# Kernel optimization log

Hardware: AMD Instinct MI355X
Metric: run time of the kernel (lower is better)

## Reference

```python
import jax, jax.numpy as jnp
import numpy as np

N_NODES = 100000


def gcn_conv(x, src, dst, W, b, n_nodes):
    # PyG GCNConv: add self-loops, sym-normalize, transform then aggregate.
    loop = jnp.arange(n_nodes, dtype=src.dtype)
    s = jnp.concatenate([src, loop])
    d = jnp.concatenate([dst, loop])
    ones = jnp.ones(s.shape[0], dtype=x.dtype)
    deg = jax.ops.segment_sum(ones, d, num_segments=n_nodes)
    dinv = jnp.where(deg > 0, jax.lax.rsqrt(deg), 0.0)
    norm = dinv[s] * dinv[d]  # [E+N]
    h = x @ W                 # [N, out]
    msg = h[s] * norm[:, None]
    out = jax.ops.segment_sum(msg, d, num_segments=n_nodes)
    return out + b


def setup_inputs() -> dict:
    key = jax.random.key(0)
    ks = jax.random.split(key, 10)
    n, f = N_NODES, 128
    x = jax.random.normal(ks[0], (n, f), dtype=jnp.float32)
    edge_index = jax.random.randint(ks[1], (2, 1600000), 0, n, dtype=jnp.int64)

    def glorot(k, fin, fout):
        lim = float(np.sqrt(6.0 / (fin + fout)))
        return jax.random.uniform(k, (fin, fout), jnp.float32, -lim, lim)

    return {
        "x": x,
        "edge_index": edge_index,
        "W1": glorot(ks[2], f, 128), "b1": jnp.zeros((128,), jnp.float32),
        "W2": glorot(ks[3], 128, 64), "b2": jnp.zeros((64,), jnp.float32),
        "W3": glorot(ks[4], 64, 32), "b3": jnp.zeros((32,), jnp.float32),
        "Wc": glorot(ks[5], 64, 1), "bc": jnp.zeros((1,), jnp.float32),
    }


def reference(x, edge_index, W1, b1, W2, b2, W3, b3, Wc, bc):
    n = x.shape[0]
    src, dst = edge_index[0], edge_index[1]
    h = jax.nn.relu(gcn_conv(x, src, dst, W1, b1, n))   # dropout: eval mode
    h = jax.nn.relu(gcn_conv(h, src, dst, W2, b2, n))
    h = jax.nn.relu(gcn_conv(h, src, dst, W3, b3, n))
    edge_feat = jnp.concatenate([h[src], h[dst]], axis=1)  # [E, 64]
    return edge_feat @ Wc + bc
```

## Files before the change

### kernel.cpp

```cpp
#include <hip/hip_runtime.h>


typedef unsigned short u16;
typedef short bfrag __attribute__((ext_vector_type(8)));
typedef float ffrag __attribute__((ext_vector_type(4)));

#define BSHIFT 8
#define MAXB   512
#define BIN_CHUNK 4096
#define BCAP   4608

static __device__ __forceinline__ float4 f4add(float4 a, float4 b) {
    return make_float4(a.x + b.x, a.y + b.y, a.z + b.z, a.w + b.w);
}

static __device__ __forceinline__ u16 f2bf(float f) {
    unsigned u = __float_as_uint(f);
    u = (u + 0x7FFFu + ((u >> 16) & 1u)) >> 16;
    return (u16)u;
}

static __device__ __forceinline__ float bflo(unsigned u) {
    return __uint_as_float(u << 16);
}
static __device__ __forceinline__ float bfhi(unsigned u) {
    return __uint_as_float(u & 0xFFFF0000u);
}
static __device__ __forceinline__ void bfacc2(float& a0, float& a1, unsigned u) {
    a0 += bflo(u);
    a1 += bfhi(u);
}


__global__ __launch_bounds__(256) void bin_edges(const int* __restrict__ src,
                                                 const int* __restrict__ dst,
                                                 int* __restrict__ bcur,
                                                 unsigned* __restrict__ pairs,
                                                 int E, int B) {
    __shared__ int h[MAXB];
    __shared__ int base[MAXB];
    const int t = threadIdx.x;
    const int e0 = blockIdx.x * BIN_CHUNK;
    const int eEnd = min(e0 + BIN_CHUNK, E);
    for (int i = t; i < B; i += 256) h[i] = 0;
    __syncthreads();
    for (int e = e0 + t; e < eEnd; e += 256)
        atomicAdd(&h[dst[e] >> BSHIFT], 1);
    __syncthreads();
    for (int i = t; i < B; i += 256) {
        int c = h[i];
        base[i] = c ? atomicAdd(&bcur[i], c) : 0;
        h[i] = 0;
    }
    __syncthreads();
    for (int e = e0 + t; e < eEnd; e += 256) {
        int d = dst[e];
        int b = d >> BSHIFT;
        int pos = base[b] + atomicAdd(&h[b], 1);
        pairs[pos] = ((unsigned)(d & 255) << 24) | (unsigned)src[e];
    }
}

__global__ __launch_bounds__(256) void build_csr(const unsigned* __restrict__ pairs,
                                                 const int* __restrict__ bcur,
                                                 int* __restrict__ rowp,
                                                 int* __restrict__ rowe,
                                                 float* __restrict__ dinv,
                                                 int* __restrict__ ssrc, int N) {
    __shared__ int s[256];
    __shared__ int cur[256];
    const int t = threadIdx.x;
    const int b = blockIdx.x;
    const int eBeg = b * BCAP, eEnd = bcur[b];
    const int nodeBase = b << BSHIFT;
    s[t] = 0;
    __syncthreads();
    for (int e = eBeg + t; e < eEnd; e += 256)
        atomicAdd(&s[pairs[e] >> 24], 1);
    __syncthreads();
    const int v = s[t];
    #pragma unroll
    for (int off = 1; off < 256; off <<= 1) {
        int add = (t >= off) ? s[t - off] : 0;
        __syncthreads();
        s[t] += add;
        __syncthreads();
    }
    const int rp = eBeg + s[t] - v;
    const int node = nodeBase + t;
    if (node < N) {
        rowp[node] = rp;
        rowe[node] = rp + v;
        dinv[node] = rsqrtf((float)(v + 1));
    }
    cur[t] = rp;
    __syncthreads();
    for (int e = eBeg + t; e < eEnd; e += 256) {
        unsigned p = pairs[e];
        int pos = atomicAdd(&cur[p >> 24], 1);
        ssrc[pos] = (int)(p & 0xFFFFFFu);
    }
}

__global__ __launch_bounds__(256) void prep_all(const float* __restrict__ W1,
                                                u16* __restrict__ w1t,
                                                const float* __restrict__ W2,
                                                u16* __restrict__ w2t,
                                                int* __restrict__ bcur, int B) {
    int idx = blockIdx.x * 256 + threadIdx.x;
    if (idx < 128 * 128) {
        int n = idx >> 7, k = idx & 127;
        w1t[idx] = f2bf(W1[k * 128 + n]);
    } else if (idx < 128 * 128 + 64 * 128) {
        int j = idx - 128 * 128;
        int n = j >> 7, k = j & 127;
        w2t[j] = f2bf(W2[k * 64 + n]);
    }
    if (idx < B) bcur[idx] = idx * BCAP;
}

template <int FIN, int FOUT, bool AF32, int MINW>
__global__ __launch_bounds__(256, MINW)
void gemm_mfma(const void* __restrict__ Xv, const u16* __restrict__ Wt,
               const float* __restrict__ dinv, u16* __restrict__ G, int N) {
    constexpr int NT = FOUT / 16;
    constexpr int KK = FIN / 32;
    constexpr int CB = FIN / 8;
    constexpr int ITER = (64 * CB) / 256;
    __shared__ __align__(16) u16 xs[64 * FIN];
    __shared__ float ldv[64];

    const int t = threadIdx.x;
    const int wave = t >> 6;
    const int lane = t & 63;
    const int l15 = lane & 15;
    const int quad = lane >> 4;
    const int r0 = blockIdx.x * 64;

    bfrag Bf[NT][KK];
    #pragma unroll
    for (int nt = 0; nt < NT; nt++)
        #pragma unroll
        for (int kk = 0; kk < KK; kk++)
            Bf[nt][kk] = *reinterpret_cast<const bfrag*>(
                &Wt[(size_t)(nt * 16 + l15) * FIN + kk * 32 + quad * 8]);

    if (t < 64) ldv[t] = (r0 + t < N) ? dinv[r0 + t] : 0.f;

    #pragma unroll
    for (int i = 0; i < ITER; i++) {
        int v = t + 256 * i;
        int row = v / CB;
        int cb = v - row * CB;
        uint4 pack = make_uint4(0, 0, 0, 0);
        if (r0 + row < N) {
            if (AF32) {
                const float* X = (const float*)Xv;
                const float4* p = reinterpret_cast<const float4*>(
                    &X[(size_t)(r0 + row) * FIN + cb * 8]);
                float4 lo = p[0], hi = p[1];
                pack.x = f2bf(lo.x) | ((unsigned)f2bf(lo.y) << 16);
                pack.y = f2bf(lo.z) | ((unsigned)f2bf(lo.w) << 16);
                pack.z = f2bf(hi.x) | ((unsigned)f2bf(hi.y) << 16);
                pack.w = f2bf(hi.z) | ((unsigned)f2bf(hi.w) << 16);
            } else {
                const u16* X = (const u16*)Xv;
                pack = *reinterpret_cast<const uint4*>(
                    &X[(size_t)(r0 + row) * FIN + cb * 8]);
            }
        }
        int cbs = cb ^ (row & 7);
        *reinterpret_cast<uint4*>(&xs[row * FIN + cbs * 8]) = pack;
    }
    __syncthreads();

    ffrag acc[NT];
    #pragma unroll
    for (int nt = 0; nt < NT; nt++) {
        acc[nt][0] = 0.f; acc[nt][1] = 0.f; acc[nt][2] = 0.f; acc[nt][3] = 0.f;
    }

    const int arow = wave * 16 + l15;
    #pragma unroll
    for (int kk = 0; kk < KK; kk++) {
        int cb = (kk * 4 + quad) ^ (l15 & 7);
        bfrag a = *reinterpret_cast<const bfrag*>(&xs[arow * FIN + cb * 8]);
        #pragma unroll
        for (int nt = 0; nt < NT; nt++)
            acc[nt] = __builtin_amdgcn_mfma_f32_16x16x32_bf16(a, Bf[nt][kk], acc[nt], 0, 0, 0);
    }

    #pragma unroll
    for (int nt = 0; nt < NT; nt++)
        #pragma unroll
        for (int r = 0; r < 4; r++) {
            int rl = wave * 16 + quad * 4 + r;
            int grow = r0 + rl;
            if (grow < N)
                G[(size_t)grow * FOUT + nt * 16 + l15] = f2bf(acc[nt][r] * ldv[rl]);
        }
}

__global__ __launch_bounds__(256) void agg1_gemm2(const u16* __restrict__ G,
                                                  const int* __restrict__ rowp,
                                                  const int* __restrict__ rowe,
                                                  const int* __restrict__ ssrc,
                                                  const float* __restrict__ dinv,
                                                  const float* __restrict__ bias,
                                                  const u16* __restrict__ w2t,
                                                  u16* __restrict__ g2, int N) {
    __shared__ __align__(16) u16 hl[16][136];
    __shared__ float ldv[16];
    const int t = threadIdx.x;
    const int wave = t >> 6;
    const int lane = t & 63;
    const int l15 = lane & 15;
    const int quad = lane >> 4;
    const int lj = t & 15;
    const int dn = t >> 4;
    const int d0 = blockIdx.x * 16;
    const int d = d0 + dn;

    bfrag Bf[4];
    #pragma unroll
    for (int kk = 0; kk < 4; kk++)
        Bf[kk] = *reinterpret_cast<const bfrag*>(
            &w2t[(size_t)(wave * 16 + l15) * 128 + kk * 32 + quad * 8]);

    if (t < 16) ldv[t] = (d0 + t < N) ? dinv[d0 + t] : 0.f;

    uint4 pk = make_uint4(0, 0, 0, 0);
    if (d < N) {
        const uint4* G4 = reinterpret_cast<const uint4*>(G);
        float a[8];
        #pragma unroll
        for (int i = 0; i < 8; i++) a[i] = 0.f;
        {
            uint4 u = G4[(size_t)d * 16 + lj];
            bfacc2(a[0], a[1], u.x); bfacc2(a[2], a[3], u.y);
            bfacc2(a[4], a[5], u.z); bfacc2(a[6], a[7], u.w);
        }
        int e = rowp[d];
        const int end = rowe[d];
        for (; e + 4 <= end; e += 4) {
            int s0 = ssrc[e], s1 = ssrc[e + 1], s2 = ssrc[e + 2], s3 = ssrc[e + 3];
            uint4 u0 = G4[(size_t)s0 * 16 + lj];
            uint4 u1 = G4[(size_t)s1 * 16 + lj];
            uint4 u2 = G4[(size_t)s2 * 16 + lj];
            uint4 u3 = G4[(size_t)s3 * 16 + lj];
            bfacc2(a[0], a[1], u0.x); bfacc2(a[2], a[3], u0.y);
            bfacc2(a[4], a[5], u0.z); bfacc2(a[6], a[7], u0.w);
            bfacc2(a[0], a[1], u1.x); bfacc2(a[2], a[3], u1.y);
            bfacc2(a[4], a[5], u1.z); bfacc2(a[6], a[7], u1.w);
            bfacc2(a[0], a[1], u2.x); bfacc2(a[2], a[3], u2.y);
            bfacc2(a[4], a[5], u2.z); bfacc2(a[6], a[7], u2.w);
            bfacc2(a[0], a[1], u3.x); bfacc2(a[2], a[3], u3.y);
            bfacc2(a[4], a[5], u3.z); bfacc2(a[6], a[7], u3.w);
        }
        for (; e < end; e++) {
            uint4 u = G4[(size_t)ssrc[e] * 16 + lj];
            bfacc2(a[0], a[1], u.x); bfacc2(a[2], a[3], u.y);
            bfacc2(a[4], a[5], u.z); bfacc2(a[6], a[7], u.w);
        }
        const float dv = ldv[dn];
        const float4 b0 = reinterpret_cast<const float4*>(bias)[lj * 2];
        const float4 b1 = reinterpret_cast<const float4*>(bias)[lj * 2 + 1];
        float h[8];
        h[0] = fmaxf(a[0] * dv + b0.x, 0.f);
        h[1] = fmaxf(a[1] * dv + b0.y, 0.f);
        h[2] = fmaxf(a[2] * dv + b0.z, 0.f);
        h[3] = fmaxf(a[3] * dv + b0.w, 0.f);
        h[4] = fmaxf(a[4] * dv + b1.x, 0.f);
        h[5] = fmaxf(a[5] * dv + b1.y, 0.f);
        h[6] = fmaxf(a[6] * dv + b1.z, 0.f);
        h[7] = fmaxf(a[7] * dv + b1.w, 0.f);
        pk.x = f2bf(h[0]) | ((unsigned)f2bf(h[1]) << 16);
        pk.y = f2bf(h[2]) | ((unsigned)f2bf(h[3]) << 16);
        pk.z = f2bf(h[4]) | ((unsigned)f2bf(h[5]) << 16);
        pk.w = f2bf(h[6]) | ((unsigned)f2bf(h[7]) << 16);
    }
    *reinterpret_cast<uint4*>(&hl[dn][lj * 8]) = pk;
    __syncthreads();

    ffrag acc;
    acc[0] = 0.f; acc[1] = 0.f; acc[2] = 0.f; acc[3] = 0.f;
    #pragma unroll
    for (int kk = 0; kk < 4; kk++) {
        bfrag av = *reinterpret_cast<const bfrag*>(&hl[l15][kk * 32 + quad * 8]);
        acc = __builtin_amdgcn_mfma_f32_16x16x32_bf16(av, Bf[kk], acc, 0, 0, 0);
    }
    #pragma unroll
    for (int r = 0; r < 4; r++) {
        int row = quad * 4 + r;
        int node = d0 + row;
        if (node < N)
            g2[(size_t)node * 64 + wave * 16 + l15] = f2bf(acc[r] * ldv[row]);
    }
}

__global__ __launch_bounds__(256) void agg2_gemm3(const u16* __restrict__ G,
                                                  const int* __restrict__ rowp,
                                                  const int* __restrict__ rowe,
                                                  const int* __restrict__ ssrc,
                                                  const float* __restrict__ dinv,
                                                  const float* __restrict__ bias,
                                                  const float* __restrict__ W3,
                                                  float* __restrict__ g3, int N) {
    __shared__ __align__(16) float wl[64 * 32];
    __shared__ __align__(16) float hl[32][68];
    const int t = threadIdx.x;
    {
        const float4* s4 = reinterpret_cast<const float4*>(W3);
        float4* d4 = reinterpret_cast<float4*>(wl);
        d4[t] = s4[t];
        d4[t + 256] = s4[t + 256];
    }
    __syncthreads();
    const int lj = t & 7;
    const int dn = t >> 3;
    const int d = blockIdx.x * 32 + dn;
    if (d >= N) return;

    const uint4* G4 = reinterpret_cast<const uint4*>(G);
    float a[8];
    #pragma unroll
    for (int i = 0; i < 8; i++) a[i] = 0.f;
    {
        uint4 u = G4[(size_t)d * 8 + lj];
        bfacc2(a[0], a[1], u.x); bfacc2(a[2], a[3], u.y);
        bfacc2(a[4], a[5], u.z); bfacc2(a[6], a[7], u.w);
    }
    int e = rowp[d];
    const int end = rowe[d];
    for (; e + 4 <= end; e += 4) {
        int s0 = ssrc[e], s1 = ssrc[e + 1], s2 = ssrc[e + 2], s3 = ssrc[e + 3];
        uint4 u0 = G4[(size_t)s0 * 8 + lj];
        uint4 u1 = G4[(size_t)s1 * 8 + lj];
        uint4 u2 = G4[(size_t)s2 * 8 + lj];
        uint4 u3 = G4[(size_t)s3 * 8 + lj];
        bfacc2(a[0], a[1], u0.x); bfacc2(a[2], a[3], u0.y);
        bfacc2(a[4], a[5], u0.z); bfacc2(a[6], a[7], u0.w);
        bfacc2(a[0], a[1], u1.x); bfacc2(a[2], a[3], u1.y);
        bfacc2(a[4], a[5], u1.z); bfacc2(a[6], a[7], u1.w);
        bfacc2(a[0], a[1], u2.x); bfacc2(a[2], a[3], u2.y);
        bfacc2(a[4], a[5], u2.z); bfacc2(a[6], a[7], u2.w);
        bfacc2(a[0], a[1], u3.x); bfacc2(a[2], a[3], u3.y);
        bfacc2(a[4], a[5], u3.z); bfacc2(a[6], a[7], u3.w);
    }
    for (; e < end; e++) {
        uint4 u = G4[(size_t)ssrc[e] * 8 + lj];
        bfacc2(a[0], a[1], u.x); bfacc2(a[2], a[3], u.y);
        bfacc2(a[4], a[5], u.z); bfacc2(a[6], a[7], u.w);
    }
    const float dv = dinv[d];
    const float4 b0 = reinterpret_cast<const float4*>(bias)[lj * 2];
    const float4 b1 = reinterpret_cast<const float4*>(bias)[lj * 2 + 1];
    float h[8];
    h[0] = fmaxf(a[0] * dv + b0.x, 0.f);
    h[1] = fmaxf(a[1] * dv + b0.y, 0.f);
    h[2] = fmaxf(a[2] * dv + b0.z, 0.f);
    h[3] = fmaxf(a[3] * dv + b0.w, 0.f);
    h[4] = fmaxf(a[4] * dv + b1.x, 0.f);
    h[5] = fmaxf(a[5] * dv + b1.y, 0.f);
    h[6] = fmaxf(a[6] * dv + b1.z, 0.f);
    h[7] = fmaxf(a[7] * dv + b1.w, 0.f);
    *reinterpret_cast<float4*>(&hl[dn][lj * 8])     = make_float4(h[0], h[1], h[2], h[3]);
    *reinterpret_cast<float4*>(&hl[dn][lj * 8 + 4]) = make_float4(h[4], h[5], h[6], h[7]);
    float g[4] = {0.f, 0.f, 0.f, 0.f};
    #pragma unroll 4
    for (int k4 = 0; k4 < 16; k4++) {
        float4 hv = *reinterpret_cast<const float4*>(&hl[dn][k4 * 4]);
        float hs[4] = {hv.x, hv.y, hv.z, hv.w};
        #pragma unroll
        for (int p = 0; p < 4; p++) {
            float4 w = *reinterpret_cast<const float4*>(&wl[(k4 * 4 + p) * 32 + lj * 4]);
            g[0] += hs[p] * w.x; g[1] += hs[p] * w.y;
            g[2] += hs[p] * w.z; g[3] += hs[p] * w.w;
        }
    }
    *reinterpret_cast<float4*>(&g3[(size_t)d * 32 + lj * 4]) =
        make_float4(g[0] * dv, g[1] * dv, g[2] * dv, g[3] * dv);
}

__global__ __launch_bounds__(256) void aggregate_l3s(const float* __restrict__ G,
                                                     const int* __restrict__ rowp,
                                                     const int* __restrict__ rowe,
                                                     const int* __restrict__ ssrc,
                                                     const float* __restrict__ dinv,
                                                     const float* __restrict__ bias,
                                                     const float* __restrict__ Wc,
                                                     float2* __restrict__ ab, int N) {
    constexpr int L = 8;
    const int t = threadIdx.x;
    const int lj = t % L;
    const int d = blockIdx.x * 32 + t / L;
    if (d >= N) return;

    const float4* G4 = reinterpret_cast<const float4*>(G);
    float4 acc = G4[(size_t)d * L + lj];
    int e = rowp[d];
    const int end = rowe[d];
    for (; e + 4 <= end; e += 4) {
        int s0 = ssrc[e], s1 = ssrc[e + 1], s2 = ssrc[e + 2], s3 = ssrc[e + 3];
        float4 v0 = G4[(size_t)s0 * L + lj];
        float4 v1 = G4[(size_t)s1 * L + lj];
        float4 v2 = G4[(size_t)s2 * L + lj];
        float4 v3 = G4[(size_t)s3 * L + lj];
        acc = f4add(acc, f4add(f4add(v0, v1), f4add(v2, v3)));
    }
    for (; e < end; e++)
        acc = f4add(acc, G4[(size_t)ssrc[e] * L + lj]);
    const float dv = dinv[d];
    const float4 b4 = reinterpret_cast<const float4*>(bias)[lj];
    float4 h;
    h.x = fmaxf(acc.x * dv + b4.x, 0.f);
    h.y = fmaxf(acc.y * dv + b4.y, 0.f);
    h.z = fmaxf(acc.z * dv + b4.z, 0.f);
    h.w = fmaxf(acc.w * dv + b4.w, 0.f);
    const float4 wa = reinterpret_cast<const float4*>(Wc)[lj];
    const float4 wb = reinterpret_cast<const float4*>(Wc + 32)[lj];
    float p = h.x * wa.x + h.y * wa.y + h.z * wa.z + h.w * wa.w;
    float q = h.x * wb.x + h.y * wb.y + h.z * wb.z + h.w * wb.w;
    p += __shfl_xor(p, 1); q += __shfl_xor(q, 1);
    p += __shfl_xor(p, 2); q += __shfl_xor(q, 2);
    p += __shfl_xor(p, 4); q += __shfl_xor(q, 4);
    if (lj == 0) ab[d] = make_float2(p, q);
}


__global__ __launch_bounds__(256) void edge_out(const int* __restrict__ src,
                                                const int* __restrict__ dst,
                                                const float2* __restrict__ ab,
                                                const float* __restrict__ bc,
                                                float* __restrict__ out, int E) {
    int e = blockIdx.x * 256 + threadIdx.x;
    if (e < E) out[e] = ab[src[e]].x + ab[dst[e]].y + bc[0];
}

extern "C" void kernel_launch(void* const* d_in, const int* in_sizes, int n_in,
                              void* d_out, int out_size, void* d_ws, size_t ws_size,
                              hipStream_t stream) {
    const float* x  = (const float*)d_in[0];
    const int*   ei = (const int*)d_in[1];
    const float* W1 = (const float*)d_in[2];
    const float* b1 = (const float*)d_in[3];
    const float* W2 = (const float*)d_in[4];
    const float* b2 = (const float*)d_in[5];
    const float* W3 = (const float*)d_in[6];
    const float* b3 = (const float*)d_in[7];
    const float* Wc = (const float*)d_in[8];
    const float* bc = (const float*)d_in[9];
    float* out = (float*)d_out;

    const int N = in_sizes[0] / 128;
    const int E = in_sizes[1] / 2;
    const int B = (N + 255) >> BSHIFT;
    const int* src = ei;
    const int* dst = ei + E;

    size_t off = 0;
    auto alloc = [&](size_t bytes) -> void* {
        size_t o = (off + 255) & ~(size_t)255;
        off = o + bytes;
        return (void*)((char*)d_ws + o);
    };
    float* dinv = (float*)alloc((size_t)N * 4);
    int*   rowp = (int*)alloc((size_t)N * 4);
    int*   rowe = (int*)alloc((size_t)N * 4);
    int*   bcur = (int*)alloc((size_t)(B + 1) * 4);
    int*   ssrc = (int*)alloc((size_t)B * BCAP * 4);
    u16*   w1t  = (u16*)alloc(128 * 128 * 2);
    u16*   w2t  = (u16*)alloc(64 * 128 * 2);
    u16*   g16  = (u16*)alloc((size_t)N * 128 * 2);
    u16*   g2b  = (u16*)alloc((size_t)N * 64 * 2);
    float2* ab  = (float2*)alloc((size_t)N * 8);
    (void)ws_size; (void)n_in; (void)out_size;

    unsigned* pairs = (unsigned*)g2b;
    float* g3f = (float*)g16;

    const int gE = (E + 255) / 256;
    const int gR = (N + 63) / 64;

    prep_all<<<96, 256, 0, stream>>>(W1, w1t, W2, w2t, bcur, B);
    bin_edges<<<(E + BIN_CHUNK - 1) / BIN_CHUNK, 256, 0, stream>>>(src, dst, bcur, pairs, E, B);
    build_csr<<<B, 256, 0, stream>>>(pairs, bcur, rowp, rowe, dinv, ssrc, N);

    gemm_mfma<128, 128, true, 2><<<gR, 256, 0, stream>>>(x, w1t, dinv, g16, N);
    agg1_gemm2<<<(N + 15) / 16, 256, 0, stream>>>(g16, rowp, rowe, ssrc, dinv, b1, w2t, g2b, N);
    agg2_gemm3<<<(N + 31) / 32, 256, 0, stream>>>(g2b, rowp, rowe, ssrc, dinv, b2, W3, g3f, N);
    aggregate_l3s<<<(N + 31) / 32, 256, 0, stream>>>(g3f, rowp, rowe, ssrc, dinv, b3, Wc, ab, N);

    edge_out<<<gE, 256, 0, stream>>>(src, dst, ab, bc, out, E);
}
```

Before: 319.8 us.

## Sort nodes by degree within each bin to balance aggregation waves

build_csr now computes a per-bin permutation of nodes, counting-sorted by in-degree with the degree key capped at 63, and writes -1 for padding slots. The three aggregation kernels map each thread group to a node through this permutation, so the threads of one wavefront handle nodes of similar degree and diverge less in their gather loops. The gather loops also gain an 8-way unrolled stage to keep more loads in flight. The cost is an extra indirection load per node, scattered output writes, a serial 64-entry scan on one thread per bin, and higher register pressure from the wider unroll.

```diff
diff --git a/kernel.cpp b/kernel.cpp
--- a/kernel.cpp
+++ b/kernel.cpp
@@ -29,6 +29,10 @@
 static __device__ __forceinline__ void bfacc2(float& a0, float& a1, unsigned u) {
     a0 += bflo(u);
     a1 += bfhi(u);
+}
+static __device__ __forceinline__ void bfacc8(float* a, uint4 u) {
+    bfacc2(a[0], a[1], u.x); bfacc2(a[2], a[3], u.y);
+    bfacc2(a[4], a[5], u.z); bfacc2(a[6], a[7], u.w);
 }
 
 
@@ -66,14 +70,17 @@
                                                  int* __restrict__ rowp,
                                                  int* __restrict__ rowe,
                                                  float* __restrict__ dinv,
-                                                 int* __restrict__ ssrc, int N) {
+                                                 int* __restrict__ ssrc,
+                                                 int* __restrict__ perm, int N) {
     __shared__ int s[256];
     __shared__ int cur[256];
+    __shared__ int hcur[64];
     const int t = threadIdx.x;
     const int b = blockIdx.x;
     const int eBeg = b * BCAP, eEnd = bcur[b];
     const int nodeBase = b << BSHIFT;
     s[t] = 0;
+    if (t < 64) hcur[t] = 0;
     __syncthreads();
     for (int e = eBeg + t; e < eEnd; e += 256)
         atomicAdd(&s[pairs[e] >> 24], 1);
@@ -88,13 +95,28 @@
     }
     const int rp = eBeg + s[t] - v;
     const int node = nodeBase + t;
-    if (node < N) {
+    const int nvalid = min(N - nodeBase, 256);
+    const int dc = min(v, 63);
+    if (t < nvalid) {
         rowp[node] = rp;
         rowe[node] = rp + v;
         dinv[node] = rsqrtf((float)(v + 1));
+        atomicAdd(&hcur[dc], 1);
+    } else {
+        perm[(b << 8) + t] = -1;
     }
     cur[t] = rp;
     __syncthreads();
+    if (t == 0) {
+        int acc = 0;
+        #pragma unroll
+        for (int i = 0; i < 64; i++) { int h = hcur[i]; hcur[i] = acc; acc += h; }
+    }
+    __syncthreads();
+    if (t < nvalid) {
+        int rank = atomicAdd(&hcur[dc], 1);
+        perm[(b << 8) + rank] = node;
+    }
     for (int e = eBeg + t; e < eEnd; e += 256) {
         unsigned p = pairs[e];
         int pos = atomicAdd(&cur[p >> 24], 1);
@@ -205,12 +227,14 @@
                                                   const int* __restrict__ rowp,
                                                   const int* __restrict__ rowe,
                                                   const int* __restrict__ ssrc,
+                                                  const int* __restrict__ perm,
                                                   const float* __restrict__ dinv,
                                                   const float* __restrict__ bias,
                                                   const u16* __restrict__ w2t,
                                                   u16* __restrict__ g2, int N) {
     __shared__ __align__(16) u16 hl[16][136];
     __shared__ float ldv[16];
+    __shared__ int pn[16];
     const int t = threadIdx.x;
     const int wave = t >> 6;
     const int lane = t & 63;
@@ -219,50 +243,48 @@
     const int lj = t & 15;
     const int dn = t >> 4;
     const int d0 = blockIdx.x * 16;
-    const int d = d0 + dn;
-
-    bfrag Bf[4];
-    #pragma unroll
-    for (int kk = 0; kk < 4; kk++)
-        Bf[kk] = *reinterpret_cast<const bfrag*>(
-            &w2t[(size_t)(wave * 16 + l15) * 128 + kk * 32 + quad * 8]);
-
-    if (t < 16) ldv[t] = (d0 + t < N) ? dinv[d0 + t] : 0.f;
+
+    if (t < 16) {
+        int nd = perm[d0 + t];
+        pn[t] = nd;
+        ldv[t] = (nd >= 0) ? dinv[nd] : 0.f;
+    }
+    const int d = perm[d0 + dn];
 
     uint4 pk = make_uint4(0, 0, 0, 0);
-    if (d < N) {
+    if (d >= 0) {
         const uint4* G4 = reinterpret_cast<const uint4*>(G);
         float a[8];
         #pragma unroll
         for (int i = 0; i < 8; i++) a[i] = 0.f;
-        {
-            uint4 u = G4[(size_t)d * 16 + lj];
-            bfacc2(a[0], a[1], u.x); bfacc2(a[2], a[3], u.y);
-            bfacc2(a[4], a[5], u.z); bfacc2(a[6], a[7], u.w);
-        }
+        bfacc8(a, G4[(size_t)d * 16 + lj]);
         int e = rowp[d];
         const int end = rowe[d];
+        for (; e + 8 <= end; e += 8) {
+            int s0 = ssrc[e],     s1 = ssrc[e + 1], s2 = ssrc[e + 2], s3 = ssrc[e + 3];
+            int s4 = ssrc[e + 4], s5 = ssrc[e + 5], s6 = ssrc[e + 6], s7 = ssrc[e + 7];
+            uint4 u0 = G4[(size_t)s0 * 16 + lj];
+            uint4 u1 = G4[(size_t)s1 * 16 + lj];
+            uint4 u2 = G4[(size_t)s2 * 16 + lj];
+            uint4 u3 = G4[(size_t)s3 * 16 + lj];
+            uint4 u4 = G4[(size_t)s4 * 16 + lj];
+            uint4 u5 = G4[(size_t)s5 * 16 + lj];
+            uint4 u6 = G4[(size_t)s6 * 16 + lj];
+            uint4 u7 = G4[(size_t)s7 * 16 + lj];
+            bfacc8(a, u0); bfacc8(a, u1); bfacc8(a, u2); bfacc8(a, u3);
+            bfacc8(a, u4); bfacc8(a, u5); bfacc8(a, u6); bfacc8(a, u7);
+        }
         for (; e + 4 <= end; e += 4) {
             int s0 = ssrc[e], s1 = ssrc[e + 1], s2 = ssrc[e + 2], s3 = ssrc[e + 3];
             uint4 u0 = G4[(size_t)s0 * 16 + lj];
             uint4 u1 = G4[(size_t)s1 * 16 + lj];
             uint4 u2 = G4[(size_t)s2 * 16 + lj];
             uint4 u3 = G4[(size_t)s3 * 16 + lj];
-            bfacc2(a[0], a[1], u0.x); bfacc2(a[2], a[3], u0.y);
-            bfacc2(a[4], a[5], u0.z); bfacc2(a[6], a[7], u0.w);
-            bfacc2(a[0], a[1], u1.x); bfacc2(a[2], a[3], u1.y);
-            bfacc2(a[4], a[5], u1.z); bfacc2(a[6], a[7], u1.w);
-            bfacc2(a[0], a[1], u2.x); bfacc2(a[2], a[3], u2.y);
-            bfacc2(a[4], a[5], u2.z); bfacc2(a[6], a[7], u2.w);
-            bfacc2(a[0], a[1], u3.x); bfacc2(a[2], a[3], u3.y);
-            bfacc2(a[4], a[5], u3.z); bfacc2(a[6], a[7], u3.w);
+            bfacc8(a, u0); bfacc8(a, u1); bfacc8(a, u2); bfacc8(a, u3);
         }
-        for (; e < end; e++) {
-            uint4 u = G4[(size_t)ssrc[e] * 16 + lj];
-            bfacc2(a[0], a[1], u.x); bfacc2(a[2], a[3], u.y);
-            bfacc2(a[4], a[5], u.z); bfacc2(a[6], a[7], u.w);
-        }
-        const float dv = ldv[dn];
+        for (; e < end; e++)
+            bfacc8(a, G4[(size_t)ssrc[e] * 16 + lj]);
+        const float dv = dinv[d];
         const float4 b0 = reinterpret_cast<const float4*>(bias)[lj * 2];
         const float4 b1 = reinterpret_cast<const float4*>(bias)[lj * 2 + 1];
         float h[8];
@@ -282,6 +304,12 @@
     *reinterpret_cast<uint4*>(&hl[dn][lj * 8]) = pk;
     __syncthreads();
 
+    bfrag Bf[4];
+    #pragma unroll
+    for (int kk = 0; kk < 4; kk++)
+        Bf[kk] = *reinterpret_cast<const bfrag*>(
+            &w2t[(size_t)(wave * 16 + l15) * 128 + kk * 32 + quad * 8]);
+
     ffrag acc;
     acc[0] = 0.f; acc[1] = 0.f; acc[2] = 0.f; acc[3] = 0.f;
     #pragma unroll
@@ -292,8 +320,8 @@
     #pragma unroll
     for (int r = 0; r < 4; r++) {
         int row = quad * 4 + r;
-        int node = d0 + row;
-        if (node < N)
+        int node = pn[row];
+        if (node >= 0)
             g2[(size_t)node * 64 + wave * 16 + l15] = f2bf(acc[r] * ldv[row]);
     }
 }
@@ -302,6 +330,7 @@
                                                   const int* __restrict__ rowp,
                                                   const int* __restrict__ rowe,
                                                   const int* __restrict__ ssrc,
+                                                  const int* __restrict__ perm,
                                                   const float* __restrict__ dinv,
                                                   const float* __restrict__ bias,
                                                   const float* __restrict__ W3,
@@ -318,40 +347,40 @@
     __syncthreads();
     const int lj = t & 7;
     const int dn = t >> 3;
-    const int d = blockIdx.x * 32 + dn;
-    if (d >= N) return;
+    const int d = perm[blockIdx.x * 32 + dn];
+    if (d < 0) return;
 
     const uint4* G4 = reinterpret_cast<const uint4*>(G);
     float a[8];
     #pragma unroll
     for (int i = 0; i < 8; i++) a[i] = 0.f;
-    {
-        uint4 u = G4[(size_t)d * 8 + lj];
-        bfacc2(a[0], a[1], u.x); bfacc2(a[2], a[3], u.y);
-        bfacc2(a[4], a[5], u.z); bfacc2(a[6], a[7], u.w);
-    }
+    bfacc8(a, G4[(size_t)d * 8 + lj]);
     int e = rowp[d];
     const int end = rowe[d];
+    for (; e + 8 <= end; e += 8) {
+        int s0 = ssrc[e],     s1 = ssrc[e + 1], s2 = ssrc[e + 2], s3 = ssrc[e + 3];
+        int s4 = ssrc[e + 4], s5 = ssrc[e + 5], s6 = ssrc[e + 6], s7 = ssrc[e + 7];
+        uint4 u0 = G4[(size_t)s0 * 8 + lj];
+        uint4 u1 = G4[(size_t)s1 * 8 + lj];
+        uint4 u2 = G4[(size_t)s2 * 8 + lj];
+        uint4 u3 = G4[(size_t)s3 * 8 + lj];
+        uint4 u4 = G4[(size_t)s4 * 8 + lj];
+        uint4 u5 = G4[(size_t)s5 * 8 + lj];
+        uint4 u6 = G4[(size_t)s6 * 8 + lj];
+        uint4 u7 = G4[(size_t)s7 * 8 + lj];
+        bfacc8(a, u0); bfacc8(a, u1); bfacc8(a, u2); bfacc8(a, u3);
+        bfacc8(a, u4); bfacc8(a, u5); bfacc8(a, u6); bfacc8(a, u7);
+    }
     for (; e + 4 <= end; e += 4) {
         int s0 = ssrc[e], s1 = ssrc[e + 1], s2 = ssrc[e + 2], s3 = ssrc[e + 3];
         uint4 u0 = G4[(size_t)s0 * 8 + lj];
         uint4 u1 = G4[(size_t)s1 * 8 + lj];
         uint4 u2 = G4[(size_t)s2 * 8 + lj];
         uint4 u3 = G4[(size_t)s3 * 8 + lj];
-        bfacc2(a[0], a[1], u0.x); bfacc2(a[2], a[3], u0.y);
-        bfacc2(a[4], a[5], u0.z); bfacc2(a[6], a[7], u0.w);
-        bfacc2(a[0], a[1], u1.x); bfacc2(a[2], a[3], u1.y);
-        bfacc2(a[4], a[5], u1.z); bfacc2(a[6], a[7], u1.w);
-        bfacc2(a[0], a[1], u2.x); bfacc2(a[2], a[3], u2.y);
-        bfacc2(a[4], a[5], u2.z); bfacc2(a[6], a[7], u2.w);
-        bfacc2(a[0], a[1], u3.x); bfacc2(a[2], a[3], u3.y);
-        bfacc2(a[4], a[5], u3.z); bfacc2(a[6], a[7], u3.w);
-    }
-    for (; e < end; e++) {
-        uint4 u = G4[(size_t)ssrc[e] * 8 + lj];
-        bfacc2(a[0], a[1], u.x); bfacc2(a[2], a[3], u.y);
-        bfacc2(a[4], a[5], u.z); bfacc2(a[6], a[7], u.w);
-    }
+        bfacc8(a, u0); bfacc8(a, u1); bfacc8(a, u2); bfacc8(a, u3);
+    }
+    for (; e < end; e++)
+        bfacc8(a, G4[(size_t)ssrc[e] * 8 + lj]);
     const float dv = dinv[d];
     const float4 b0 = reinterpret_cast<const float4*>(bias)[lj * 2];
     const float4 b1 = reinterpret_cast<const float4*>(bias)[lj * 2 + 1];
@@ -386,6 +415,7 @@
                                                      const int* __restrict__ rowp,
                                                      const int* __restrict__ rowe,
                                                      const int* __restrict__ ssrc,
+                                                     const int* __restrict__ perm,
                                                      const float* __restrict__ dinv,
                                                      const float* __restrict__ bias,
                                                      const float* __restrict__ Wc,
@@ -393,13 +423,27 @@
     constexpr int L = 8;
     const int t = threadIdx.x;
     const int lj = t % L;
-    const int d = blockIdx.x * 32 + t / L;
-    if (d >= N) return;
+    const int d = perm[blockIdx.x * 32 + t / L];
+    if (d < 0) return;
 
     const float4* G4 = reinterpret_cast<const float4*>(G);
     float4 acc = G4[(size_t)d * L + lj];
     int e = rowp[d];
     const int end = rowe[d];
+    for (; e + 8 <= end; e += 8) {
+        int s0 = ssrc[e],     s1 = ssrc[e + 1], s2 = ssrc[e + 2], s3 = ssrc[e + 3];
+        int s4 = ssrc[e + 4], s5 = ssrc[e + 5], s6 = ssrc[e + 6], s7 = ssrc[e + 7];
+        float4 v0 = G4[(size_t)s0 * L + lj];
+        float4 v1 = G4[(size_t)s1 * L + lj];
+        float4 v2 = G4[(size_t)s2 * L + lj];
+        float4 v3 = G4[(size_t)s3 * L + lj];
+        float4 v4 = G4[(size_t)s4 * L + lj];
+        float4 v5 = G4[(size_t)s5 * L + lj];
+        float4 v6 = G4[(size_t)s6 * L + lj];
+        float4 v7 = G4[(size_t)s7 * L + lj];
+        acc = f4add(acc, f4add(f4add(f4add(v0, v1), f4add(v2, v3)),
+                               f4add(f4add(v4, v5), f4add(v6, v7))));
+    }
     for (; e + 4 <= end; e += 4) {
         int s0 = ssrc[e], s1 = ssrc[e + 1], s2 = ssrc[e + 2], s3 = ssrc[e + 3];
         float4 v0 = G4[(size_t)s0 * L + lj];
@@ -469,6 +513,7 @@
     int*   rowe = (int*)alloc((size_t)N * 4);
     int*   bcur = (int*)alloc((size_t)(B + 1) * 4);
     int*   ssrc = (int*)alloc((size_t)B * BCAP * 4);
+    int*   perm = (int*)alloc((size_t)B * 256 * 4);
     u16*   w1t  = (u16*)alloc(128 * 128 * 2);
     u16*   w2t  = (u16*)alloc(64 * 128 * 2);
     u16*   g16  = (u16*)alloc((size_t)N * 128 * 2);
@@ -484,12 +529,12 @@
 
     prep_all<<<96, 256, 0, stream>>>(W1, w1t, W2, w2t, bcur, B);
     bin_edges<<<(E + BIN_CHUNK - 1) / BIN_CHUNK, 256, 0, stream>>>(src, dst, bcur, pairs, E, B);
-    build_csr<<<B, 256, 0, stream>>>(pairs, bcur, rowp, rowe, dinv, ssrc, N);
+    build_csr<<<B, 256, 0, stream>>>(pairs, bcur, rowp, rowe, dinv, ssrc, perm, N);
 
     gemm_mfma<128, 128, true, 2><<<gR, 256, 0, stream>>>(x, w1t, dinv, g16, N);
-    agg1_gemm2<<<(N + 15) / 16, 256, 0, stream>>>(g16, rowp, rowe, ssrc, dinv, b1, w2t, g2b, N);
-    agg2_gemm3<<<(N + 31) / 32, 256, 0, stream>>>(g2b, rowp, rowe, ssrc, dinv, b2, W3, g3f, N);
-    aggregate_l3s<<<(N + 31) / 32, 256, 0, stream>>>(g3f, rowp, rowe, ssrc, dinv, b3, Wc, ab, N);
+    agg1_gemm2<<<B * 16, 256, 0, stream>>>(g16, rowp, rowe, ssrc, perm, dinv, b1, w2t, g2b, N);
+    agg2_gemm3<<<B * 8, 256, 0, stream>>>(g2b, rowp, rowe, ssrc, perm, dinv, b2, W3, g3f, N);
+    aggregate_l3s<<<B * 8, 256, 0, stream>>>(g3f, rowp, rowe, ssrc, perm, dinv, b3, Wc, ab, N);
 
     edge_out<<<gE, 256, 0, stream>>>(src, dst, ab, bc, out, E);
 }
```

New measurement: 342.9 us. +7.2%, slower.
